# Optimization experiments

Measured on AMD Instinct MI355X. Metric: run time of the kernel, lower is better.

## Reference

```python
import jax, jax.numpy as jnp
import numpy as np


def setup_inputs() -> dict:
    key = jax.random.key(0)
    k1, k2, k3, k4 = jax.random.split(key, 4)
    bs, ch, T = 8, 256, 512
    N, P = 2048, 16
    feat = jax.random.normal(k1, (bs, ch, T), dtype=jnp.float32)
    # rois: [N, 3] = (batch_idx, start, end) in feature coordinates
    bidx = jax.random.randint(k2, (N,), 0, bs).astype(jnp.float32)
    u1 = jax.random.uniform(k3, (N,), dtype=jnp.float32)
    u2 = jax.random.uniform(k4, (N,), dtype=jnp.float32)
    start = u1 * (T - 1)
    end = start + u2 * (T - start)
    rois = jnp.stack([bidx, start, end], axis=1).astype(jnp.float32)
    return {"input": feat, "rois": rois, "feature_dim": P, "ratio": 4}


def reference(input, rois, feature_dim, ratio):
    # 1D ROI Align: input [bs, ch, T], rois [N, 3]=(batch_idx, start, end)
    # -> output [N, ch, feature_dim]
    bs, ch, T = input.shape
    bidx = rois[:, 0].astype(jnp.int32)              # [N]
    start = rois[:, 1]
    end = rois[:, 2]
    roi_len = jnp.maximum(end - start, 1.0)          # malformed ROI guard
    bin_size = roi_len / feature_dim                 # [N]
    S = ratio                                        # samples per bin (static)
    p = jnp.arange(feature_dim, dtype=jnp.float32)   # bin index
    s = (jnp.arange(S, dtype=jnp.float32) + 0.5) / S # fractional offset in bin
    # sample coordinates x: [N, P, S]
    x = start[:, None, None] + (p[None, :, None] + s[None, None, :]) * bin_size[:, None, None]
    valid = (x >= -1.0) & (x <= T)                   # out-of-range samples -> 0
    xc = jnp.clip(x, 0.0, T - 1)
    x_low = jnp.floor(xc).astype(jnp.int32)
    x_high = jnp.minimum(x_low + 1, T - 1)
    lx = xc - x_low.astype(jnp.float32)              # linear interp weight
    b = bidx[:, None, None]                          # [N,1,1]
    v_low = input[b, :, x_low]                       # [N, P, S, ch]
    v_high = input[b, :, x_high]                     # [N, P, S, ch]
    val = v_low * (1.0 - lx[..., None]) + v_high * lx[..., None]
    val = jnp.where(valid[..., None], val, 0.0)
    out = val.mean(axis=2)                           # average over samples -> [N, P, ch]
    return jnp.transpose(out, (0, 2, 1))             # [N, ch, P]
```

## Files before the change

kernel.cpp:

```cpp
#include <hip/hip_runtime.h>


#define T_DIM 512
#define CH    256
#define P_DIM 16
#define S_RAT 4
#define CTILE 8
#define NCT   (CH / CTILE)
#define RSPLIT 8
#define MAXSL  256
#define MAXMETA 96
#define TSTRIDE 520

typedef _Float16 h2 __attribute__((ext_vector_type(2)));

__device__ __forceinline__ float dot2_acc(h2 a, h2 b, float c) {
#if __has_builtin(__builtin_amdgcn_fdot2)
    return __builtin_amdgcn_fdot2(a, b, c, false);
#else
    return fmaf((float)a.x, (float)b.x, fmaf((float)a.y, (float)b.y, c));
#endif
}

__global__ __launch_bounds__(256) void roialign_lds_kernel(
    const float* __restrict__ feat,
    const float* __restrict__ rois,
    float* __restrict__ out,
    int N)
{
    __shared__ __align__(16) unsigned tile[CTILE * TSTRIDE];
    __shared__ float4 s_meta[MAXMETA];
    __shared__ int    s_cnt;

    const int ct  = blockIdx.x;
    const int r   = blockIdx.y;
    const int b   = blockIdx.z;
    const int tid = threadIdx.x;

    if (tid == 0) s_cnt = 0;

    {
        const int c = tid >> 5;
        const int q = tid & 31;
        const float* srow = feat + ((size_t)b * CH + ct * CTILE + c) * T_DIM;
        const float4* src = (const float4*)srow;
        unsigned* drow = &tile[c * TSTRIDE];
        const float sc = 1.0f / S_RAT;
#pragma unroll
        for (int k = 0; k < 4; ++k) {
            const int idx = q + 32 * k;
            float4 v = src[idx];
            const int o = 4 * idx;
            float v4 = (o + 4 < T_DIM) ? srow[o + 4] : v.w;
            union { h2 h; unsigned u; } p0, p1, p2, p3;
            p0.h = h2{(_Float16)(v.x * sc), (_Float16)(v.y * sc)};
            p1.h = h2{(_Float16)(v.y * sc), (_Float16)(v.z * sc)};
            p2.h = h2{(_Float16)(v.z * sc), (_Float16)(v.w * sc)};
            p3.h = h2{(_Float16)(v.w * sc), (_Float16)(v4  * sc)};
            *(uint4*)(drow + o) = make_uint4(p0.u, p1.u, p2.u, p3.u);
        }
    }
    __syncthreads();

    {
        const int i = r * MAXSL + tid;
        if (i < N) {
            float bf = rois[3 * i];
            if ((int)bf == b) {
                int pos = atomicAdd(&s_cnt, 1);
                if (pos < MAXMETA)
                    s_meta[pos] = make_float4((float)i, rois[3 * i + 1], rois[3 * i + 2], 0.0f);
            }
        }
    }
    __syncthreads();
    const int cnt = min(s_cnt, MAXMETA);

    const int rs = tid >> 4;
    const int p  = tid & 15;

    float qf[S_RAT];
#pragma unroll
    for (int s = 0; s < S_RAT; ++s)
        qf[s] = (float)p + ((float)s + 0.5f) * (1.0f / S_RAT);

    for (int base = 0; base < cnt; base += 16) {
        const int i = base + rs;
        if (i >= cnt) break;

        const float4 m     = s_meta[i];
        const float  start = m.y;
        const float  bin   = fmaxf(m.z - start, 1.0f) * (1.0f / P_DIM);

        int t[S_RAT];
        h2  wp[S_RAT];
#pragma unroll
        for (int s = 0; s < S_RAT; ++s) {
            float x  = fmaf(qf[s], bin, start);
            float xc = fminf(x, (float)(T_DIM - 1));
            float tf = fminf(truncf(xc), (float)(T_DIM - 2));
            t[s] = (int)tf;
            float w = xc - tf;
            wp[s] = h2{(_Float16)(1.0f - w), (_Float16)w};
        }

        float* outn = out + (size_t)(int)m.x * (CH * P_DIM) + ct * (CTILE * P_DIM) + p;
#pragma unroll
        for (int c = 0; c < CTILE; ++c) {
            const unsigned* trow = &tile[c * TSTRIDE];
            float acc = 0.0f;
#pragma unroll
            for (int s = 0; s < S_RAT; ++s) {
                union { unsigned u; h2 h; } cv;
                cv.u = trow[t[s]];
                acc = dot2_acc(cv.h, wp[s], acc);
            }
            outn[c * P_DIM] = acc;
        }
    }
}

extern "C" void kernel_launch(void* const* d_in, const int* in_sizes, int n_in,
                              void* d_out, int out_size, void* d_ws, size_t ws_size,
                              hipStream_t stream) {
    const float* feat = (const float*)d_in[0];
    const float* rois = (const float*)d_in[1];
    float* out = (float*)d_out;
    const int N = in_sizes[1] / 3;

    dim3 grid(NCT, RSPLIT, 8);
    roialign_lds_kernel<<<grid, dim3(256), 0, stream>>>(feat, rois, out, N);
}
```

Baseline: 77.12 us.

## Interleave 4 channels per LDS word, ballot-compact ROIs, overlap global loads

Reorganizes the LDS tile so each 16-byte entry holds the fp16 pairs for four channels at one time index, split into four phase planes by t mod 4. Each sample then needs one 128-bit LDS read per four channels instead of one 32-bit read per channel. Global feature loads are issued before the ROI compaction so their latency overlaps that work. ROI compaction now uses a wave ballot plus one atomic per wave instead of one atomic per thread. The cost is more registers for the held loads and a bespoke barrier sequence.

```diff
diff --git a/kernel.cpp b/kernel.cpp
--- a/kernel.cpp
+++ b/kernel.cpp
@@ -10,7 +10,6 @@
 #define RSPLIT 8
 #define MAXSL  256
 #define MAXMETA 96
-#define TSTRIDE 520
 
 typedef _Float16 h2 __attribute__((ext_vector_type(2)));
 
@@ -22,13 +21,19 @@
 #endif
 }
 
+__device__ __forceinline__ unsigned pack2(float a, float b) {
+    union { h2 h; unsigned u; } u;
+    u.h = h2{(_Float16)a, (_Float16)b};
+    return u.u;
+}
+
 __global__ __launch_bounds__(256) void roialign_lds_kernel(
     const float* __restrict__ feat,
     const float* __restrict__ rois,
     float* __restrict__ out,
     int N)
 {
-    __shared__ __align__(16) unsigned tile[CTILE * TSTRIDE];
+    __shared__ __align__(16) uint4 tile[2 * T_DIM];
     __shared__ float4 s_meta[MAXMETA];
     __shared__ int    s_cnt;
 
@@ -37,41 +42,67 @@
     const int b   = blockIdx.z;
     const int tid = threadIdx.x;
 
+    const int q = tid >> 7;
+    const int k = tid & 127;
+    float4 v0, v1, v2, v3;
+    float  n0, n1, n2, n3;
+    {
+        const float* base = feat + ((size_t)b * CH + ct * CTILE + 4 * q) * T_DIM;
+        const int nidx = (4 * k + 4 < T_DIM) ? (4 * k + 4) : (T_DIM - 1);
+        v0 = ((const float4*)(base + 0 * T_DIM))[k];  n0 = (base + 0 * T_DIM)[nidx];
+        v1 = ((const float4*)(base + 1 * T_DIM))[k];  n1 = (base + 1 * T_DIM)[nidx];
+        v2 = ((const float4*)(base + 2 * T_DIM))[k];  n2 = (base + 2 * T_DIM)[nidx];
+        v3 = ((const float4*)(base + 3 * T_DIM))[k];  n3 = (base + 3 * T_DIM)[nidx];
+    }
+
     if (tid == 0) s_cnt = 0;
-
-    {
-        const int c = tid >> 5;
-        const int q = tid & 31;
-        const float* srow = feat + ((size_t)b * CH + ct * CTILE + c) * T_DIM;
-        const float4* src = (const float4*)srow;
-        unsigned* drow = &tile[c * TSTRIDE];
-        const float sc = 1.0f / S_RAT;
-#pragma unroll
-        for (int k = 0; k < 4; ++k) {
-            const int idx = q + 32 * k;
-            float4 v = src[idx];
-            const int o = 4 * idx;
-            float v4 = (o + 4 < T_DIM) ? srow[o + 4] : v.w;
-            union { h2 h; unsigned u; } p0, p1, p2, p3;
-            p0.h = h2{(_Float16)(v.x * sc), (_Float16)(v.y * sc)};
-            p1.h = h2{(_Float16)(v.y * sc), (_Float16)(v.z * sc)};
-            p2.h = h2{(_Float16)(v.z * sc), (_Float16)(v.w * sc)};
-            p3.h = h2{(_Float16)(v.w * sc), (_Float16)(v4  * sc)};
-            *(uint4*)(drow + o) = make_uint4(p0.u, p1.u, p2.u, p3.u);
-        }
-    }
-    __syncthreads();
+    asm volatile("s_waitcnt lgkmcnt(0)" ::: "memory");
+    __builtin_amdgcn_s_barrier();
+    asm volatile("" ::: "memory");
 
     {
         const int i = r * MAXSL + tid;
+        bool match = false;
+        float sx = 0.0f, ex = 0.0f;
         if (i < N) {
             float bf = rois[3 * i];
-            if ((int)bf == b) {
-                int pos = atomicAdd(&s_cnt, 1);
-                if (pos < MAXMETA)
-                    s_meta[pos] = make_float4((float)i, rois[3 * i + 1], rois[3 * i + 2], 0.0f);
-            }
+            sx = rois[3 * i + 1];
+            ex = rois[3 * i + 2];
+            match = ((int)bf == b);
         }
+        unsigned long long mask = __ballot(match);
+        const int lane = tid & 63;
+        const int pre = __popcll(mask & ((1ull << lane) - 1ull));
+        const int tot = __popcll(mask);
+        int wbase = 0;
+        if (lane == 0 && tot) wbase = atomicAdd(&s_cnt, tot);
+        wbase = __shfl(wbase, 0);
+        if (match) {
+            const int pos = wbase + pre;
+            if (pos < MAXMETA)
+                s_meta[pos] = make_float4((float)i, sx, ex, 0.0f);
+        }
+    }
+
+    {
+        const float sc = 1.0f / S_RAT;
+        uint4* trow = &tile[q * T_DIM];
+        trow[0 * 128 + k] = make_uint4(pack2(v0.x * sc, v0.y * sc),
+                                       pack2(v1.x * sc, v1.y * sc),
+                                       pack2(v2.x * sc, v2.y * sc),
+                                       pack2(v3.x * sc, v3.y * sc));
+        trow[1 * 128 + k] = make_uint4(pack2(v0.y * sc, v0.z * sc),
+                                       pack2(v1.y * sc, v1.z * sc),
+                                       pack2(v2.y * sc, v2.z * sc),
+                                       pack2(v3.y * sc, v3.z * sc));
+        trow[2 * 128 + k] = make_uint4(pack2(v0.z * sc, v0.w * sc),
+                                       pack2(v1.z * sc, v1.w * sc),
+                                       pack2(v2.z * sc, v2.w * sc),
+                                       pack2(v3.z * sc, v3.w * sc));
+        trow[3 * 128 + k] = make_uint4(pack2(v0.w * sc, n0 * sc),
+                                       pack2(v1.w * sc, n1 * sc),
+                                       pack2(v2.w * sc, n2 * sc),
+                                       pack2(v3.w * sc, n3 * sc));
     }
     __syncthreads();
     const int cnt = min(s_cnt, MAXMETA);
@@ -84,38 +115,47 @@
     for (int s = 0; s < S_RAT; ++s)
         qf[s] = (float)p + ((float)s + 0.5f) * (1.0f / S_RAT);
 
-    for (int base = 0; base < cnt; base += 16) {
-        const int i = base + rs;
+    const char* tbase = (const char*)tile;
+
+    for (int base2 = 0; base2 < cnt; base2 += 16) {
+        const int i = base2 + rs;
         if (i >= cnt) break;
 
         const float4 m     = s_meta[i];
         const float  start = m.y;
         const float  bin   = fmaxf(m.z - start, 1.0f) * (1.0f / P_DIM);
 
-        int t[S_RAT];
+        int boff[S_RAT];
         h2  wp[S_RAT];
 #pragma unroll
         for (int s = 0; s < S_RAT; ++s) {
             float x  = fmaf(qf[s], bin, start);
             float xc = fminf(x, (float)(T_DIM - 1));
             float tf = fminf(truncf(xc), (float)(T_DIM - 2));
-            t[s] = (int)tf;
-            float w = xc - tf;
-            wp[s] = h2{(_Float16)(1.0f - w), (_Float16)w};
+            const int t = (int)tf;
+            const float w = xc - tf;
+            wp[s]   = h2{(_Float16)(1.0f - w), (_Float16)w};
+            boff[s] = ((t & 3) << 11) | ((t >> 2) << 4);
         }
 
         float* outn = out + (size_t)(int)m.x * (CH * P_DIM) + ct * (CTILE * P_DIM) + p;
 #pragma unroll
-        for (int c = 0; c < CTILE; ++c) {
-            const unsigned* trow = &tile[c * TSTRIDE];
-            float acc = 0.0f;
+        for (int qq = 0; qq < 2; ++qq) {
+            float a0 = 0.0f, a1 = 0.0f, a2 = 0.0f, a3 = 0.0f;
 #pragma unroll
             for (int s = 0; s < S_RAT; ++s) {
-                union { unsigned u; h2 h; } cv;
-                cv.u = trow[t[s]];
-                acc = dot2_acc(cv.h, wp[s], acc);
+                const uint4 e = *(const uint4*)(tbase + qq * 8192 + boff[s]);
+                union { unsigned u; h2 h; } c0, c1, c2, c3;
+                c0.u = e.x; c1.u = e.y; c2.u = e.z; c3.u = e.w;
+                a0 = dot2_acc(c0.h, wp[s], a0);
+                a1 = dot2_acc(c1.h, wp[s], a1);
+                a2 = dot2_acc(c2.h, wp[s], a2);
+                a3 = dot2_acc(c3.h, wp[s], a3);
             }
-            outn[c * P_DIM] = acc;
+            outn[(4 * qq + 0) * P_DIM] = a0;
+            outn[(4 * qq + 1) * P_DIM] = a1;
+            outn[(4 * qq + 2) * P_DIM] = a2;
+            outn[(4 * qq + 3) * P_DIM] = a3;
         }
     }
 }
```

Result: faster. 74.54 us (-3.3%).
